# Performance work log

Hardware: AMD Instinct MI355X
Metric: run time of the kernel (lower is better)

## Reference

```python
import jax, jax.numpy as jnp
import numpy as np

ALPHA = 0.95   # membrane decay
VTH = 1.0      # firing threshold
BN_EPS = 1e-5
SS_BETA = 10.0  # SuperSpike surrogate slope (used in bwd module)


def _spike(v):
    # Heaviside spike on (v - vth) already subtracted
    return (v > 0).astype(v.dtype)


def _batchnorm(h, scale, bias):
    # per-timestep batch norm over the batch axis (train mode, batch stats)
    mu = jnp.mean(h, axis=0, keepdims=True)
    var = jnp.mean(jnp.square(h - mu), axis=0, keepdims=True)
    return (h - mu) * jax.lax.rsqrt(var + BN_EPS) * scale + bias


def _lif_layer(x, W, scale=None, bias=None):
    # x: [T, B, F_in] -> spikes z: [T, B, F_out]
    T, B, _ = x.shape
    F_out = W.shape[1]
    I = jnp.einsum('tbf,fo->tbo', x, W)  # precompute dense projection for all steps

    def step(v, i_t):
        if scale is not None:
            i_t = _batchnorm(i_t, scale, bias)
        v = ALPHA * v + i_t
        z = _spike(v - VTH)
        v = v * (1.0 - z)  # reset-to-zero
        return v, z

    v0 = jnp.zeros((B, F_out), dtype=x.dtype)
    _, z = jax.lax.scan(step, v0, I)
    return z


def setup_inputs() -> dict:
    key = jax.random.key(0)
    k1, k2, k3 = jax.random.split(key, 3)
    B, T, H, Wd, C = 512, 100, 28, 28, 2
    inputs = jax.random.uniform(k1, (B, T, H, Wd, C), dtype=jnp.float32)
    trgt = jax.random.randint(k2, (B,), 0, 10)
    W1 = jax.random.normal(k3, (784, 100), dtype=jnp.float32) * (1.0 / np.sqrt(784))
    bn_scale = jnp.ones((100,), dtype=jnp.float32)
    bn_bias = jnp.zeros((100,), dtype=jnp.float32)
    W2 = jax.random.normal(jax.random.fold_in(key, 7), (100, 10), dtype=jnp.float32) * (1.0 / np.sqrt(100))
    return {"inputs": inputs, "trgt": trgt, "W1": W1, "bn_scale": bn_scale,
            "bn_bias": bn_bias, "W2": W2}


def reference(inputs, trgt, W1, bn_scale, bn_bias, W2):
    # inputs: [B, T, H, W, C]
    x = jnp.mean(inputs, axis=-1, keepdims=True)        # [B,T,H,W,1]
    x = jnp.swapaxes(x, 0, 1)                            # [T,B,H,W,1]
    x = jnp.reshape(x, (x.shape[0], x.shape[1], -1))     # [T,B,784]
    z1 = _lif_layer(x, W1, bn_scale, bn_bias)            # [T,B,100]
    z2 = _lif_layer(z1, W2)                              # [T,B,10]
    out = jnp.mean(z2, axis=0)                           # [B,10]
    return out
```

## Files before the change

kernel.cpp:

```cpp
#include <hip/hip_runtime.h>

#define T_STEPS 100
#define BATCH   512
#define FIN     784
#define O1      100
#define O2      10
#define KC1     28
#define NC1     (FIN / KC1)

typedef __attribute__((ext_vector_type(4))) double f64x4;

__device__ __forceinline__ void block_sync_lds() {
  __builtin_amdgcn_sched_barrier(0);
  asm volatile("s_waitcnt lgkmcnt(0)" ::: "memory");
  __builtin_amdgcn_s_barrier();
  __builtin_amdgcn_sched_barrier(0);
}

__global__ __launch_bounds__(256, 4) void k1_mfma(const float* __restrict__ in,
                                                  const float* __restrict__ W1,
                                                  double* __restrict__ I1T) {
  __shared__ double AI[KC1][34];
  const int tid = threadIdx.x;
  const int l   = tid & 63;
  const int w   = tid >> 6;
  const int wb  = w & 1;
  const int wo  = w >> 1;
  const int r16 = l & 15;
  const int q16 = l >> 4;
  const int b0  = (int)blockIdx.x * 32;
  const int t   = (int)blockIdx.y;

  bool iact[2]; int irow[2], iq[2]; const float* ibp[2];
#pragma unroll
  for (int p = 0; p < 2; ++p) {
    const int i = p * 256 + tid;
    iact[p] = (i < 448);
    irow[p] = iact[p] ? i / 14 : 0;
    iq[p]   = i - irow[p] * 14;
    ibp[p]  = in + ((size_t)(b0 + irow[p]) * T_STEPS + t) * (FIN * 2) + iq[p] * 4;
  }

  float4 ist[2];
#pragma unroll
  for (int p = 0; p < 2; ++p) if (iact[p]) ist[p] = *reinterpret_cast<const float4*>(ibp[p]);

  const f64x4 z = {0.0, 0.0, 0.0, 0.0};
  f64x4 pr = __builtin_amdgcn_mfma_f64_16x16x4f64((double)r16, 0.25, z, 0, 0, 0);
  f64x4 pc = __builtin_amdgcn_mfma_f64_16x16x4f64(0.25, (double)r16, z, 0, 0, 0);
  int rmv[4], cmv[4];
#pragma unroll
  for (int r = 0; r < 4; ++r) {
    int rm = (int)(pr[r] + 0.5); rmv[r] = rm < 0 ? 0 : (rm > 15 ? 15 : rm);
    int cm = (int)(pc[r] + 0.5); cmv[r] = cm < 0 ? 0 : (cm > 15 ? 15 : cm);
  }

  f64x4 acc0 = {0.0, 0.0, 0.0, 0.0};
  f64x4 acc1 = {0.0, 0.0, 0.0, 0.0};
  f64x4 acc2 = {0.0, 0.0, 0.0, 0.0};
  f64x4 acc3 = {0.0, 0.0, 0.0, 0.0};

  const float* pW0 = W1 + (size_t)q16 * O1 + r16 + (wo ? 64 : 0);

  for (int c = 0; c < NC1; ++c) {
    block_sync_lds();
#pragma unroll
    for (int p = 0; p < 2; ++p)
      if (iact[p]) {
        AI[iq[p] * 2 + 0][irow[p]] = 0.5 * ((double)ist[p].x + (double)ist[p].y);
        AI[iq[p] * 2 + 1][irow[p]] = 0.5 * ((double)ist[p].z + (double)ist[p].w);
      }
    float wreg[7][4];
    const float* pWc = pW0 + (size_t)c * (KC1 * O1);
    if (wo == 0) {
#pragma unroll
      for (int q = 0; q < 7; ++q) {
        wreg[q][0] = pWc[q * 400 +  0];
        wreg[q][1] = pWc[q * 400 + 16];
        wreg[q][2] = pWc[q * 400 + 32];
        wreg[q][3] = pWc[q * 400 + 48];
      }
    } else {
#pragma unroll
      for (int q = 0; q < 7; ++q) {
        wreg[q][0] = pWc[q * 400 +  0];
        wreg[q][1] = pWc[q * 400 + 16];
        wreg[q][2] = pWc[q * 400 + 20];
      }
    }
    if (c + 1 < NC1) {
#pragma unroll
      for (int p = 0; p < 2; ++p)
        if (iact[p]) ist[p] = *reinterpret_cast<const float4*>(ibp[p] + (c + 1) * 56);
    }
    block_sync_lds();
    if (wo == 0) {
#pragma unroll
      for (int q = 0; q < 7; ++q) {
        const double bv = AI[q * 4 + q16][wb * 16 + r16];
        acc0 = __builtin_amdgcn_mfma_f64_16x16x4f64((double)wreg[q][0], bv, acc0, 0, 0, 0);
        acc1 = __builtin_amdgcn_mfma_f64_16x16x4f64((double)wreg[q][1], bv, acc1, 0, 0, 0);
        acc2 = __builtin_amdgcn_mfma_f64_16x16x4f64((double)wreg[q][2], bv, acc2, 0, 0, 0);
        acc3 = __builtin_amdgcn_mfma_f64_16x16x4f64((double)wreg[q][3], bv, acc3, 0, 0, 0);
      }
    } else {
#pragma unroll
      for (int q = 0; q < 7; ++q) {
        const double bv = AI[q * 4 + q16][wb * 16 + r16];
        acc0 = __builtin_amdgcn_mfma_f64_16x16x4f64((double)wreg[q][0], bv, acc0, 0, 0, 0);
        acc1 = __builtin_amdgcn_mfma_f64_16x16x4f64((double)wreg[q][1], bv, acc1, 0, 0, 0);
        acc2 = __builtin_amdgcn_mfma_f64_16x16x4f64((double)wreg[q][2], bv, acc2, 0, 0, 0);
      }
    }
  }

  double* base = I1T + (size_t)t * O1 * BATCH + (b0 + wb * 16);
#define STORE_TILE(ACC, O0)                                               \
  {                                                                       \
    base[(size_t)((O0) + rmv[0]) * BATCH + cmv[0]] = (ACC)[0];            \
    base[(size_t)((O0) + rmv[1]) * BATCH + cmv[1]] = (ACC)[1];            \
    base[(size_t)((O0) + rmv[2]) * BATCH + cmv[2]] = (ACC)[2];            \
    base[(size_t)((O0) + rmv[3]) * BATCH + cmv[3]] = (ACC)[3];            \
  }
  if (wo == 0) {
    STORE_TILE(acc0, 0);
    STORE_TILE(acc1, 16);
    STORE_TILE(acc2, 32);
    STORE_TILE(acc3, 48);
  } else {
    STORE_TILE(acc0, 64);
    STORE_TILE(acc1, 80);
    STORE_TILE(acc2, 84);
  }
#undef STORE_TILE
}

__global__ __launch_bounds__(256) void k2_bnstats(const double* __restrict__ I1T,
                                                  double* __restrict__ mu,
                                                  double* __restrict__ rstd) {
  const int r    = blockIdx.x * 4 + (threadIdx.x >> 6);
  const int lane = threadIdx.x & 63;
  const double2* row2 = reinterpret_cast<const double2*>(I1T + (size_t)r * BATCH) + lane * 4;
  double v[8];
#pragma unroll
  for (int u = 0; u < 4; ++u) {
    double2 p = row2[u];
    v[2 * u] = p.x; v[2 * u + 1] = p.y;
  }
  double s = 0.0;
#pragma unroll
  for (int u = 0; u < 8; ++u) s += v[u];
#pragma unroll
  for (int m = 32; m >= 1; m >>= 1) s += __shfl_xor(s, m, 64);
  const double mean = s / 512.0;
  double q = 0.0;
#pragma unroll
  for (int u = 0; u < 8; ++u) { double d = v[u] - mean; q += d * d; }
#pragma unroll
  for (int m = 32; m >= 1; m >>= 1) q += __shfl_xor(q, m, 64);
  if (lane == 0) {
    mu[r]   = mean;
    rstd[r] = 1.0 / sqrt(q / 512.0 + 1e-5);
  }
}

__global__ __launch_bounds__(512) void k3_lif1(const double* __restrict__ I1T,
                                               const double* __restrict__ mu,
                                               const double* __restrict__ rstd,
                                               const float* __restrict__ scale,
                                               const float* __restrict__ bias,
                                               float* __restrict__ z1T) {
  const int o = blockIdx.x;
  const int b = threadIdx.x;
  const double sc = (double)scale[o], bs = (double)bias[o];
  double v = 0.0;
  for (int tc = 0; tc < T_STEPS; tc += 10) {
    double x[10], muv[10], rsv[10];
#pragma unroll
    for (int u = 0; u < 10; ++u) {
      const int t = tc + u;
      x[u]   = I1T[((size_t)t * O1 + o) * BATCH + b];
      muv[u] = mu[t * O1 + o];
      rsv[u] = rstd[t * O1 + o];
    }
#pragma unroll
    for (int u = 0; u < 10; ++u) {
      const double i = ((x[u] - muv[u]) * rsv[u]) * sc + bs;
      v = 0.95 * v + i;
      const bool z = (v > 1.0);
      z1T[((size_t)(tc + u) * O1 + o) * BATCH + b] = z ? 1.0f : 0.0f;
      if (z) v = 0.0;
    }
  }
}

__global__ __launch_bounds__(512) void k4_proj2(const float* __restrict__ z1T,
                                                const float* __restrict__ W2,
                                                double* __restrict__ I2) {
  __shared__ double W2_lds[O1 * O2];
  const int t = blockIdx.x;
  const int b = threadIdx.x;
  for (int i = threadIdx.x; i < O1 * O2; i += 512) W2_lds[i] = (double)W2[i];
  __syncthreads();
  double acc[O2];
#pragma unroll
  for (int j = 0; j < O2; ++j) acc[j] = 0.0;
  for (int o = 0; o < O1; ++o) {
    const double z = (double)z1T[((size_t)t * O1 + o) * BATCH + b];
#pragma unroll
    for (int j = 0; j < O2; ++j) acc[j] += z * W2_lds[o * O2 + j];
  }
#pragma unroll
  for (int j = 0; j < O2; ++j)
    I2[((size_t)t * O2 + j) * BATCH + b] = acc[j];
}

__global__ __launch_bounds__(512) void k5_lif2(const double* __restrict__ I2,
                                               float* __restrict__ out) {
  const int j = blockIdx.x;
  const int b = threadIdx.x;
  double v = 0.0;
  int cnt = 0;
  for (int tc = 0; tc < T_STEPS; tc += 10) {
    double x[10];
#pragma unroll
    for (int u = 0; u < 10; ++u)
      x[u] = I2[((size_t)(tc + u) * O2 + j) * BATCH + b];
#pragma unroll
    for (int u = 0; u < 10; ++u) {
      v = 0.95 * v + x[u];
      if (v > 1.0) { ++cnt; v = 0.0; }
    }
  }
  out[b * O2 + j] = (float)((double)cnt / 100.0);
}

extern "C" void kernel_launch(void* const* d_in, const int* in_sizes, int n_in,
                              void* d_out, int out_size, void* d_ws, size_t ws_size,
                              hipStream_t stream) {
  const float* in    = (const float*)d_in[0];
  const float* W1    = (const float*)d_in[2];
  const float* scale = (const float*)d_in[3];
  const float* bias  = (const float*)d_in[4];
  const float* W2    = (const float*)d_in[5];
  float* out = (float*)d_out;

  char* ws = (char*)d_ws;
  size_t off = 0;
  double* I1T  = (double*)(ws + off); off += (size_t)T_STEPS * O1 * BATCH * sizeof(double);
  double* mu   = (double*)(ws + off); off += (size_t)T_STEPS * O1 * sizeof(double);
  double* rstd = (double*)(ws + off); off += (size_t)T_STEPS * O1 * sizeof(double);
  float*  z1T  = (float*)(ws + off);  off += (size_t)T_STEPS * O1 * BATCH * sizeof(float);
  double* I2   = (double*)(ws + off); off += (size_t)T_STEPS * O2 * BATCH * sizeof(double);

  k1_mfma   <<<dim3(BATCH / 32, T_STEPS), 256, 0, stream>>>(in, W1, I1T);
  k2_bnstats<<<dim3(T_STEPS * O1 / 4), 256, 0, stream>>>(I1T, mu, rstd);
  k3_lif1   <<<dim3(O1), 512, 0, stream>>>(I1T, mu, rstd, scale, bias, z1T);
  k4_proj2  <<<dim3(T_STEPS), 512, 0, stream>>>(z1T, W2, I2);
  k5_lif2   <<<dim3(O2), 512, 0, stream>>>(I2, out);
}
```

Before: 265.5 us.

## Process two timesteps per block in projection kernel to reuse W1 registers

Each k1 block now handles two timesteps for the same 32-row batch tile, so every wave computes two B-subtiles with the same W1 register fragments. This halves the W1 global loads per output and halves the grid size. The LDS staging writes are moved after the weight loads to overlap better. In exchange the kernel uses more accumulator registers and LDS, which may reduce occupancy, and there are half as many blocks to spread across the GPU.

```diff
diff --git a/kernel.cpp b/kernel.cpp
--- a/kernel.cpp
+++ b/kernel.cpp
@@ -20,56 +20,53 @@
 __global__ __launch_bounds__(256, 4) void k1_mfma(const float* __restrict__ in,
                                                   const float* __restrict__ W1,
                                                   double* __restrict__ I1T) {
-  __shared__ double AI[KC1][34];
+  __shared__ double AI[KC1][69];
   const int tid = threadIdx.x;
   const int l   = tid & 63;
   const int w   = tid >> 6;
-  const int wb  = w & 1;
+  const int wN  = w & 1;
   const int wo  = w >> 1;
   const int r16 = l & 15;
   const int q16 = l >> 4;
   const int b0  = (int)blockIdx.x * 32;
-  const int t   = (int)blockIdx.y;
-
-  bool iact[2]; int irow[2], iq[2]; const float* ibp[2];
-#pragma unroll
-  for (int p = 0; p < 2; ++p) {
+  const int t0  = (int)blockIdx.y * 2;
+
+  bool iact[4]; int irow[4], iq[4]; const float* ibp[4];
+#pragma unroll
+  for (int p = 0; p < 4; ++p) {
     const int i = p * 256 + tid;
-    iact[p] = (i < 448);
-    irow[p] = iact[p] ? i / 14 : 0;
-    iq[p]   = i - irow[p] * 14;
-    ibp[p]  = in + ((size_t)(b0 + irow[p]) * T_STEPS + t) * (FIN * 2) + iq[p] * 4;
-  }
-
-  float4 ist[2];
-#pragma unroll
-  for (int p = 0; p < 2; ++p) if (iact[p]) ist[p] = *reinterpret_cast<const float4*>(ibp[p]);
+    iact[p] = (i < 896);
+    const int nrow = iact[p] ? i / 14 : 0;
+    iq[p]   = (iact[p] ? i : 0) - nrow * 14;
+    irow[p] = nrow;
+    const int tsub = nrow >> 5, brow = nrow & 31;
+    ibp[p]  = in + ((size_t)(b0 + brow) * T_STEPS + (t0 + tsub)) * (FIN * 2) + iq[p] * 4;
+  }
+
+  float4 ist[4];
+#pragma unroll
+  for (int p = 0; p < 4; ++p) if (iact[p]) ist[p] = *reinterpret_cast<const float4*>(ibp[p]);
 
   const f64x4 z = {0.0, 0.0, 0.0, 0.0};
   f64x4 pr = __builtin_amdgcn_mfma_f64_16x16x4f64((double)r16, 0.25, z, 0, 0, 0);
   f64x4 pc = __builtin_amdgcn_mfma_f64_16x16x4f64(0.25, (double)r16, z, 0, 0, 0);
-  int rmv[4], cmv[4];
-#pragma unroll
-  for (int r = 0; r < 4; ++r) {
-    int rm = (int)(pr[r] + 0.5); rmv[r] = rm < 0 ? 0 : (rm > 15 ? 15 : rm);
-    int cm = (int)(pc[r] + 0.5); cmv[r] = cm < 0 ? 0 : (cm > 15 ? 15 : cm);
-  }
-
-  f64x4 acc0 = {0.0, 0.0, 0.0, 0.0};
-  f64x4 acc1 = {0.0, 0.0, 0.0, 0.0};
-  f64x4 acc2 = {0.0, 0.0, 0.0, 0.0};
-  f64x4 acc3 = {0.0, 0.0, 0.0, 0.0};
+  int soff0, soff1, soff2, soff3;
+  {
+    int rm0 = (int)(pr[0] + 0.5), cm0 = (int)(pc[0] + 0.5);
+    int rm1 = (int)(pr[1] + 0.5), cm1 = (int)(pc[1] + 0.5);
+    int rm2 = (int)(pr[2] + 0.5), cm2 = (int)(pc[2] + 0.5);
+    int rm3 = (int)(pr[3] + 0.5), cm3 = (int)(pc[3] + 0.5);
+    soff0 = rm0 * BATCH + cm0; soff1 = rm1 * BATCH + cm1;
+    soff2 = rm2 * BATCH + cm2; soff3 = rm3 * BATCH + cm3;
+  }
+
+  f64x4 A00 = z, A01 = z, A02 = z, A03 = z;
+  f64x4 A10 = z, A11 = z, A12 = z, A13 = z;
 
   const float* pW0 = W1 + (size_t)q16 * O1 + r16 + (wo ? 64 : 0);
 
   for (int c = 0; c < NC1; ++c) {
     block_sync_lds();
-#pragma unroll
-    for (int p = 0; p < 2; ++p)
-      if (iact[p]) {
-        AI[iq[p] * 2 + 0][irow[p]] = 0.5 * ((double)ist[p].x + (double)ist[p].y);
-        AI[iq[p] * 2 + 1][irow[p]] = 0.5 * ((double)ist[p].z + (double)ist[p].w);
-      }
     float wreg[7][4];
     const float* pWc = pW0 + (size_t)c * (KC1 * O1);
     if (wo == 0) {
@@ -88,51 +85,63 @@
         wreg[q][2] = pWc[q * 400 + 20];
       }
     }
+#pragma unroll
+    for (int p = 0; p < 4; ++p)
+      if (iact[p]) {
+        AI[iq[p] * 2 + 0][irow[p]] = 0.5 * ((double)ist[p].x + (double)ist[p].y);
+        AI[iq[p] * 2 + 1][irow[p]] = 0.5 * ((double)ist[p].z + (double)ist[p].w);
+      }
     if (c + 1 < NC1) {
 #pragma unroll
-      for (int p = 0; p < 2; ++p)
+      for (int p = 0; p < 4; ++p)
         if (iact[p]) ist[p] = *reinterpret_cast<const float4*>(ibp[p] + (c + 1) * 56);
     }
     block_sync_lds();
+#define MFMA_(D, A, B) D = __builtin_amdgcn_mfma_f64_16x16x4f64((A), (B), (D), 0, 0, 0)
     if (wo == 0) {
 #pragma unroll
       for (int q = 0; q < 7; ++q) {
-        const double bv = AI[q * 4 + q16][wb * 16 + r16];
-        acc0 = __builtin_amdgcn_mfma_f64_16x16x4f64((double)wreg[q][0], bv, acc0, 0, 0, 0);
-        acc1 = __builtin_amdgcn_mfma_f64_16x16x4f64((double)wreg[q][1], bv, acc1, 0, 0, 0);
-        acc2 = __builtin_amdgcn_mfma_f64_16x16x4f64((double)wreg[q][2], bv, acc2, 0, 0, 0);
-        acc3 = __builtin_amdgcn_mfma_f64_16x16x4f64((double)wreg[q][3], bv, acc3, 0, 0, 0);
+        const int row = q * 4 + q16;
+        const double bv0 = AI[row][wN * 32 + r16];
+        const double bv1 = AI[row][wN * 32 + 16 + r16];
+        const double w0 = (double)wreg[q][0], w1 = (double)wreg[q][1];
+        const double w2 = (double)wreg[q][2], w3 = (double)wreg[q][3];
+        MFMA_(A00, w0, bv0); MFMA_(A01, w1, bv0);
+        MFMA_(A02, w2, bv0); MFMA_(A03, w3, bv0);
+        MFMA_(A10, w0, bv1); MFMA_(A11, w1, bv1);
+        MFMA_(A12, w2, bv1); MFMA_(A13, w3, bv1);
       }
     } else {
 #pragma unroll
       for (int q = 0; q < 7; ++q) {
-        const double bv = AI[q * 4 + q16][wb * 16 + r16];
-        acc0 = __builtin_amdgcn_mfma_f64_16x16x4f64((double)wreg[q][0], bv, acc0, 0, 0, 0);
-        acc1 = __builtin_amdgcn_mfma_f64_16x16x4f64((double)wreg[q][1], bv, acc1, 0, 0, 0);
-        acc2 = __builtin_amdgcn_mfma_f64_16x16x4f64((double)wreg[q][2], bv, acc2, 0, 0, 0);
-      }
-    }
-  }
-
-  double* base = I1T + (size_t)t * O1 * BATCH + (b0 + wb * 16);
-#define STORE_TILE(ACC, O0)                                               \
-  {                                                                       \
-    base[(size_t)((O0) + rmv[0]) * BATCH + cmv[0]] = (ACC)[0];            \
-    base[(size_t)((O0) + rmv[1]) * BATCH + cmv[1]] = (ACC)[1];            \
-    base[(size_t)((O0) + rmv[2]) * BATCH + cmv[2]] = (ACC)[2];            \
-    base[(size_t)((O0) + rmv[3]) * BATCH + cmv[3]] = (ACC)[3];            \
+        const int row = q * 4 + q16;
+        const double bv0 = AI[row][wN * 32 + r16];
+        const double bv1 = AI[row][wN * 32 + 16 + r16];
+        const double w0 = (double)wreg[q][0], w1 = (double)wreg[q][1];
+        const double w2 = (double)wreg[q][2];
+        MFMA_(A00, w0, bv0); MFMA_(A01, w1, bv0); MFMA_(A02, w2, bv0);
+        MFMA_(A10, w0, bv1); MFMA_(A11, w1, bv1); MFMA_(A12, w2, bv1);
+      }
+    }
+#undef MFMA_
+  }
+
+  double* base = I1T + ((size_t)(t0 + wN) * O1) * BATCH + b0;
+#define ST(ACC, O0, BOFF)                                                  \
+  {                                                                        \
+    base[(size_t)(O0) * BATCH + (BOFF) + soff0] = (ACC)[0];                \
+    base[(size_t)(O0) * BATCH + (BOFF) + soff1] = (ACC)[1];                \
+    base[(size_t)(O0) * BATCH + (BOFF) + soff2] = (ACC)[2];                \
+    base[(size_t)(O0) * BATCH + (BOFF) + soff3] = (ACC)[3];                \
   }
   if (wo == 0) {
-    STORE_TILE(acc0, 0);
-    STORE_TILE(acc1, 16);
-    STORE_TILE(acc2, 32);
-    STORE_TILE(acc3, 48);
+    ST(A00, 0, 0);  ST(A01, 16, 0);  ST(A02, 32, 0);  ST(A03, 48, 0);
+    ST(A10, 0, 16); ST(A11, 16, 16); ST(A12, 32, 16); ST(A13, 48, 16);
   } else {
-    STORE_TILE(acc0, 64);
-    STORE_TILE(acc1, 80);
-    STORE_TILE(acc2, 84);
-  }
-#undef STORE_TILE
+    ST(A00, 64, 0);  ST(A01, 80, 0);  ST(A02, 84, 0);
+    ST(A10, 64, 16); ST(A11, 80, 16); ST(A12, 84, 16);
+  }
+#undef ST
 }
 
 __global__ __launch_bounds__(256) void k2_bnstats(const double* __restrict__ I1T,
@@ -253,7 +262,7 @@
   float*  z1T  = (float*)(ws + off);  off += (size_t)T_STEPS * O1 * BATCH * sizeof(float);
   double* I2   = (double*)(ws + off); off += (size_t)T_STEPS * O2 * BATCH * sizeof(double);
 
-  k1_mfma   <<<dim3(BATCH / 32, T_STEPS), 256, 0, stream>>>(in, W1, I1T);
+  k1_mfma   <<<dim3(BATCH / 32, T_STEPS / 2), 256, 0, stream>>>(in, W1, I1T);
   k2_bnstats<<<dim3(T_STEPS * O1 / 4), 256, 0, stream>>>(I1T, mu, rstd);
   k3_lif1   <<<dim3(O1), 512, 0, stream>>>(I1T, mu, rstd, scale, bias, z1T);
   k4_proj2  <<<dim3(T_STEPS), 512, 0, stream>>>(z1T, W2, I2);
```

New measurement: 797.0 us. +200.2%, slower.
